# Kernel optimization log

Hardware: AMD Instinct MI355X
Metric: run time of the kernel (lower is better)

Reference implementation:

```python
import jax, jax.numpy as jnp
import numpy as np

DX = 1.0
DY = 1.0
W_DIV = 1e9
W_SMOOTH = 10.0
W_STD = 100.0
EPS = 1e-10


def _corner(a, i, j, k):
    # slice dims 2,3,4: 0 -> [0:-1], 1 -> [1:]
    sl = lambda b: slice(1, None) if b else slice(0, -1)
    return a[:, :, sl(i), sl(j), sl(k)]


def setup_inputs() -> dict:
    key = jax.random.key(0)
    k1, k2 = jax.random.split(key)
    outputs = jax.random.normal(k1, (2, 1, 256, 256, 64), dtype=jnp.float32)
    targets = jax.random.normal(k2, (2, 3, 256, 256, 64), dtype=jnp.float32)
    return {"outputs": outputs, "targets": targets}


def _loss(outputs, targets):
    bx, by, bz = targets[:, 0:1], targets[:, 1:2], targets[:, 2:3]
    z = outputs[:, 0:1]

    # vertical thickness and smoothness of its square
    dz = z[..., 1:] - z[..., :-1]
    dz2 = dz ** 2
    lap = (6 * dz2[:, :, 1:-1, 1:-1, 1:-1]
           - dz2[:, :, :-2, 1:-1, 1:-1] - dz2[:, :, 2:, 1:-1, 1:-1]
           - dz2[:, :, 1:-1, :-2, 1:-1] - dz2[:, :, 1:-1, 2:, 1:-1]
           - dz2[:, :, 1:-1, 1:-1, 2:] - dz2[:, :, 1:-1, 1:-1, :-2])
    loss_smooth = jnp.mean(lap ** 2)

    # per-(batch, channel, z) std over the spatial plane (unbiased, matching torch.std)
    loss_std = jnp.mean(jnp.std(dz, axis=(2, 3), ddof=1))

    # 8 cell corners for each field
    corners = lambda a: {(i, j, k): _corner(a, i, j, k)
                         for i in (0, 1) for j in (0, 1) for k in (0, 1)}
    BX, BY, BZ, Z = corners(bx), corners(by), corners(bz), corners(z)

    az = lambda a, b: jnp.abs(Z[a] - Z[b])
    num = (0.25 * (BX[1,0,0] + BX[1,1,0] + BX[1,0,1] + BX[1,1,1]) * DY * 0.5 * (az((1,0,1),(1,0,0)) + az((1,1,1),(1,1,0)))
           - 0.25 * (BX[0,0,0] + BX[0,1,0] + BX[0,0,1] + BX[0,1,1]) * DY * 0.5 * (az((0,0,1),(0,0,0)) + az((0,1,1),(0,1,0)))
           + 0.25 * (BY[0,1,0] + BY[1,1,0] + BY[0,1,1] + BY[1,1,1]) * DX * 0.5 * (az((0,1,1),(0,1,0)) + az((1,1,1),(1,1,0)))
           - 0.25 * (BY[0,0,0] + BY[1,0,0] + BY[0,0,1] + BY[1,0,1]) * DX * 0.5 * (az((0,0,1),(0,0,0)) + az((1,0,1),(1,0,0)))
           + 0.25 * (BZ[0,0,1] + BZ[0,1,1] + BZ[1,0,1] + BZ[1,1,1]) * DX * DY
           - 0.25 * (BZ[0,0,0] + BZ[0,1,0] + BZ[1,0,0] + BZ[1,1,0]) * DX * DY
           + (BX[0,0,1] + BX[1,0,1] + BX[1,1,1]) * DY * (Z[0,0,1] - Z[1,0,1]) / 6
           + (BX[0,1,1] + BX[1,1,1] + BX[1,0,1]) * DY * (Z[0,1,1] - Z[1,1,1]) / 6
           + (BY[1,0,1] + BY[1,1,1] + BY[0,1,1]) * DX * (Z[1,0,1] - Z[1,1,1]) / 6
           + (BY[0,0,1] + BY[0,1,1] + BY[1,1,1]) * DX * (Z[0,0,1] - Z[0,1,1]) / 6
           - (BX[0,0,0] + BX[1,0,0] + BX[1,1,0]) * DY * (Z[0,0,0] - Z[1,0,0]) / 6
           - (BX[0,1,0] + BX[1,1,0] + BX[1,0,0]) * DY * (Z[0,1,0] - Z[1,1,0]) / 6
           - (BY[1,0,0] + BY[1,1,0] + BY[0,1,0]) * DX * (Z[1,0,0] - Z[1,1,0]) / 6
           - (BY[0,0,0] + BY[0,1,0] + BY[1,1,0]) * DX * (Z[0,0,0] - Z[0,1,0]) / 6)

    sum8 = lambda C: sum(C.values())
    den = ((sum8(BX) * 0.125) ** 2 + (sum8(BY) * 0.125) ** 2
           + (sum8(BZ) * 0.125) ** 2 + EPS)
    loss_div = jnp.mean(num ** 2 / den)

    return loss_div * W_DIV, loss_smooth * W_SMOOTH + loss_std * W_STD


def reference(outputs, targets):
    return _loss(outputs, targets)
```

## Files before the change

### kernel.cpp

```cpp
#include <hip/hip_runtime.h>
#include <math.h>


#define ZSTR 388
#define BSTR 324
#define BFLD 1620

__global__ __launch_bounds__(512) void zero_ws_kernel(float* ws) {
    for (int i = threadIdx.x; i < 32 * 258; i += 512) ws[i] = 0.0f;
}

#define LD5(arr, p) do { \
    float4 _a = *(const float4*)(p); float4 _b = *(const float4*)((p) + 4); \
    arr[0] = _a.x; arr[1] = _a.y; arr[2] = _a.z; arr[3] = _a.w; arr[4] = _b.x; } while (0)

__global__ __launch_bounds__(256, 4) void fused_loss_kernel(
    const float* __restrict__ zin, const float* __restrict__ tg,
    float* __restrict__ ws)
{
    __shared__ float zs[6 * ZSTR];
    __shared__ float bs[3 * BFLD];
    __shared__ float rsc[4][2];

    const int tid  = threadIdx.x;
    const int lane = tid & 63;
    const int w    = tid >> 6;

    const int bb = blockIdx.x >> 12;
    const int rest = blockIdx.x & 4095;
    const int x0 = ((rest >> 6) & 63) << 2;
    const int y0 = (rest & 63) << 2;

    const float* zg = zin + ((size_t)bb << 22);

    for (int i = tid; i < 1776; i += 256) {
        if (i < 576) {
            int row = i >> 4;
            int o   = (i & 15) << 2;
            int xi  = row / 6;
            int yr  = row - xi * 6;
            int x = x0 - 1 + xi; x = x < 0 ? 0 : (x > 255 ? 255 : x);
            int y = y0 - 1 + yr; y = y < 0 ? 0 : (y > 255 ? 255 : y);
            *(float4*)&zs[xi * ZSTR + yr * 64 + o] =
                *(const float4*)&zg[x * 16384 + y * 64 + o];
        } else {
            int j  = i - 576;
            int f  = j / 400;
            int jj = j - f * 400;
            int row = jj >> 4;
            int o   = (jj & 15) << 2;
            int xi  = row / 5;
            int yr  = row - xi * 5;
            int x = x0 + xi; x = x > 255 ? 255 : x;
            int y = y0 + yr; y = y > 255 ? 255 : y;
            const float* g = tg + ((size_t)(bb * 3 + f) << 22);
            *(float4*)&bs[f * BFLD + xi * BSTR + yr * 64 + o] =
                *(const float4*)&g[x * 16384 + y * 64 + o];
        }
    }
    __syncthreads();

    const int c  = tid >> 4;
    const int kq = tid & 15;
    const int cx = c & 3, cy = c >> 2;
    const int xg = x0 + cx, yg = y0 + cy;
    const int k0 = kq << 2;

    const float* zC = &zs[(cx + 1) * ZSTR + (cy + 1) * 64 + k0];

    float zcv[7];
    {
        float4 m = *(const float4*)(zC - 4);
        float4 a = *(const float4*)(zC);
        float4 b = *(const float4*)(zC + 4);
        zcv[0] = m.w; zcv[1] = a.x; zcv[2] = a.y; zcv[3] = a.z; zcv[4] = a.w;
        zcv[5] = b.x; zcv[6] = b.y;
    }
    float zEv[5];  LD5(zEv,  zC + ZSTR);
    float zWv[5];  LD5(zWv,  zC - ZSTR);
    float zNv[5];  LD5(zNv,  zC + 64);
    float zSv[5];  LD5(zSv,  zC - 64);
    float zNEv[5]; LD5(zNEv, zC + ZSTR + 64);

    float dz0[4], dzE[4], dzN[4], dzNE[4];
    #pragma unroll
    for (int e = 0; e < 4; ++e) {
        dz0[e]  = zcv[e + 2] - zcv[e + 1];
        dzE[e]  = zEv[e + 1] - zEv[e];
        dzN[e]  = zNv[e + 1] - zNv[e];
        dzNE[e] = zNEv[e + 1] - zNEv[e];
    }

    float s1a[4], s2a[4];
    #pragma unroll
    for (int e = 0; e < 4; ++e) {
        bool kok = (k0 + e) < 63;
        s1a[e] = kok ? dz0[e] : 0.0f;
        s2a[e] = kok ? dz0[e] * dz0[e] : 0.0f;
    }

    float sm = 0.0f;
    if (xg >= 1 && xg <= 254 && yg >= 1 && yg <= 254) {
        #pragma unroll
        for (int e = 0; e < 4; ++e) {
            int k = k0 + e;
            if (k >= 1 && k <= 61) {
                float dzm = zcv[e + 1] - zcv[e];
                float dzp = zcv[e + 3] - zcv[e + 2];
                float dzw = zWv[e + 1] - zWv[e];
                float dzs = zSv[e + 1] - zSv[e];
                float lap = 6.0f * dz0[e] * dz0[e]
                          - dzw * dzw - dzE[e] * dzE[e]
                          - dzs * dzs - dzN[e] * dzN[e]
                          - dzm * dzm - dzp * dzp;
                sm += lap * lap;
            }
        }
    }

    float dv = 0.0f;
    if (xg < 255 && yg < 255) {
        const float* bxP = &bs[cx * BSTR + cy * 64 + k0];
        const float* byP = bxP + BFLD;
        const float* bzP = byP + BFLD;
        float bx00v[5]; LD5(bx00v, bxP);
        float bx10v[5]; LD5(bx10v, bxP + BSTR);
        float bx01v[5]; LD5(bx01v, bxP + 64);
        float bx11v[5]; LD5(bx11v, bxP + BSTR + 64);
        float by00v[5]; LD5(by00v, byP);
        float by10v[5]; LD5(by10v, byP + BSTR);
        float by01v[5]; LD5(by01v, byP + 64);
        float by11v[5]; LD5(by11v, byP + BSTR + 64);
        float bz00v[5]; LD5(bz00v, bzP);
        float bz10v[5]; LD5(bz10v, bzP + BSTR);
        float bz01v[5]; LD5(bz01v, bzP + 64);
        float bz11v[5]; LD5(bz11v, bzP + BSTR + 64);

        const float c6 = 1.0f / 6.0f;
        #pragma unroll
        for (int e = 0; e < 4; ++e) {
            if ((k0 + e) < 63) {
                float adz00 = fabsf(dz0[e]),  adz10 = fabsf(dzE[e]);
                float adz01 = fabsf(dzN[e]),  adz11 = fabsf(dzNE[e]);

                float num =
                    0.125f * ( (bx10v[e] + bx10v[e+1] + bx11v[e] + bx11v[e+1]) * (adz10 + adz11)
                             - (bx00v[e] + bx00v[e+1] + bx01v[e] + bx01v[e+1]) * (adz00 + adz01)
                             + (by01v[e] + by01v[e+1] + by11v[e] + by11v[e+1]) * (adz01 + adz11)
                             - (by00v[e] + by00v[e+1] + by10v[e] + by10v[e+1]) * (adz00 + adz10) )
                  + 0.25f * ( (bz00v[e+1] + bz10v[e+1] + bz01v[e+1] + bz11v[e+1])
                            - (bz00v[e]   + bz10v[e]   + bz01v[e]   + bz11v[e]) );

                num += c6 * ( (bx00v[e+1] + bx10v[e+1] + bx11v[e+1]) * (zcv[e+2] - zEv[e+1])
                            + (bx01v[e+1] + bx11v[e+1] + bx10v[e+1]) * (zNv[e+1] - zNEv[e+1])
                            + (by10v[e+1] + by11v[e+1] + by01v[e+1]) * (zEv[e+1] - zNEv[e+1])
                            + (by00v[e+1] + by01v[e+1] + by11v[e+1]) * (zcv[e+2] - zNv[e+1])
                            - (bx00v[e] + bx10v[e] + bx11v[e]) * (zcv[e+1] - zEv[e])
                            - (bx01v[e] + bx11v[e] + bx10v[e]) * (zNv[e] - zNEv[e])
                            - (by10v[e] + by11v[e] + by01v[e]) * (zEv[e] - zNEv[e])
                            - (by00v[e] + by01v[e] + by11v[e]) * (zcv[e+1] - zNv[e]) );

                float sbx = bx00v[e] + bx00v[e+1] + bx10v[e] + bx10v[e+1]
                          + bx01v[e] + bx01v[e+1] + bx11v[e] + bx11v[e+1];
                float sby = by00v[e] + by00v[e+1] + by10v[e] + by10v[e+1]
                          + by01v[e] + by01v[e+1] + by11v[e] + by11v[e+1];
                float sbz = bz00v[e] + bz00v[e+1] + bz10v[e] + bz10v[e+1]
                          + bz01v[e] + bz01v[e+1] + bz11v[e] + bz11v[e+1];
                float den = 0.015625f * (sbx * sbx + sby * sby + sbz * sbz) + 1e-10f;
                dv += num * num / den;
            }
        }
    }

    #pragma unroll
    for (int off = 32; off > 0; off >>= 1) {
        sm += __shfl_down(sm, off, 64);
        dv += __shfl_down(dv, off, 64);
    }

    __syncthreads();
    float* r1 = zs;
    float* r2 = zs + 1024;
    { float4 v; v.x = s1a[0]; v.y = s1a[1]; v.z = s1a[2]; v.w = s1a[3];
      *(float4*)&r1[tid << 2] = v; }
    { float4 v; v.x = s2a[0]; v.y = s2a[1]; v.z = s2a[2]; v.w = s2a[3];
      *(float4*)&r2[tid << 2] = v; }
    if (lane == 0) { rsc[w][0] = sm; rsc[w][1] = dv; }
    __syncthreads();

    if (tid < 64) {
        float a = 0.0f, b2 = 0.0f;
        #pragma unroll
        for (int cc = 0; cc < 16; ++cc) {
            a  += r1[cc * 64 + tid];
            b2 += r2[cc * 64 + tid];
        }
        float* sl = ws + (blockIdx.x & 31) * 258;
        if (tid < 63) {
            atomicAdd(&sl[2 + bb * 64 + tid],   a);
            atomicAdd(&sl[130 + bb * 64 + tid], b2);
        }
        if (tid == 0) atomicAdd(&sl[0], rsc[0][0] + rsc[1][0] + rsc[2][0] + rsc[3][0]);
        if (tid == 1) atomicAdd(&sl[1], rsc[0][1] + rsc[1][1] + rsc[2][1] + rsc[3][1]);
    }
}

__global__ __launch_bounds__(128) void finalize_kernel(const float* __restrict__ ws,
                                                       float* __restrict__ out)
{
    __shared__ double red[128];
    const int t = threadIdx.x;
    double stdv = 0.0;
    {
        int k = t & 63, bb = t >> 6;
        if (k < 63) {
            double s1 = 0.0, s2 = 0.0;
            for (int p = 0; p < 32; ++p) {
                s1 += (double)ws[p * 258 + 2 + bb * 64 + k];
                s2 += (double)ws[p * 258 + 130 + bb * 64 + k];
            }
            const double N = 65536.0;
            double var = (s2 - s1 * s1 / N) / (N - 1.0);
            stdv = sqrt(var > 0.0 ? var : 0.0);
        }
    }
    red[t] = stdv;
    __syncthreads();
    for (int off = 64; off > 0; off >>= 1) {
        if (t < off) red[t] += red[t + off];
        __syncthreads();
    }
    if (t == 0) {
        double smt = 0.0, dvt = 0.0;
        for (int p = 0; p < 32; ++p) {
            smt += (double)ws[p * 258 + 0];
            dvt += (double)ws[p * 258 + 1];
        }
        double loss_std    = red[0] / 126.0;
        double loss_smooth = smt / (2.0 * 254.0 * 254.0 * 61.0);
        double loss_div    = dvt / (2.0 * 255.0 * 255.0 * 63.0);
        out[0] = (float)(loss_div * 1e9);
        out[1] = (float)(loss_smooth * 10.0 + loss_std * 100.0);
    }
}

extern "C" void kernel_launch(void* const* d_in, const int* in_sizes, int n_in,
                              void* d_out, int out_size, void* d_ws, size_t ws_size,
                              hipStream_t stream) {
    const float* z  = (const float*)d_in[0];
    const float* tg = (const float*)d_in[1];
    float* out = (float*)d_out;
    float* ws  = (float*)d_ws;

    zero_ws_kernel<<<1, 512, 0, stream>>>(ws);
    fused_loss_kernel<<<8192, 256, 0, stream>>>(z, tg, ws);
    finalize_kernel<<<1, 128, 0, stream>>>(ws, out);
}
```

Before: 206.8 us.

## Load stencil neighbours directly from global memory instead of staging tiles in LDS

Drops the shared-memory tile staging pass and its barrier. Each thread now reads its z neighbours and B-field corners straight from global memory with clamped indices, relying on L1/L2 to serve the overlapping reads. The divergence computation is split into per-field stages to cut live registers, and the divide becomes a hardware reciprocal approximation. This removes LDS traffic and a sync, but adds redundant global loads and slightly less exact division.

Measured after the change: 210.9 us. About the same (+2.0%).

```diff
diff --git a/kernel.cpp b/kernel.cpp
--- a/kernel.cpp
+++ b/kernel.cpp
@@ -2,85 +2,69 @@
 #include <math.h>
 
 
-#define ZSTR 388
-#define BSTR 324
-#define BFLD 1620
-
 __global__ __launch_bounds__(512) void zero_ws_kernel(float* ws) {
     for (int i = threadIdx.x; i < 32 * 258; i += 512) ws[i] = 0.0f;
 }
 
-#define LD5(arr, p) do { \
-    float4 _a = *(const float4*)(p); float4 _b = *(const float4*)((p) + 4); \
-    arr[0] = _a.x; arr[1] = _a.y; arr[2] = _a.z; arr[3] = _a.w; arr[4] = _b.x; } while (0)
+__device__ __forceinline__ void ld5(float* a, const float* p, int d4) {
+    float4 x = *(const float4*)p;
+    float4 y = *(const float4*)(p + d4);
+    a[0] = x.x; a[1] = x.y; a[2] = x.z; a[3] = x.w; a[4] = y.x;
+}
 
 __global__ __launch_bounds__(256, 4) void fused_loss_kernel(
     const float* __restrict__ zin, const float* __restrict__ tg,
     float* __restrict__ ws)
 {
-    __shared__ float zs[6 * ZSTR];
-    __shared__ float bs[3 * BFLD];
+    __shared__ float r1[1024];
+    __shared__ float r2[1024];
     __shared__ float rsc[4][2];
 
     const int tid  = threadIdx.x;
     const int lane = tid & 63;
     const int w    = tid >> 6;
 
-    const int bb = blockIdx.x >> 12;
+    const int bb   = blockIdx.x >> 12;
     const int rest = blockIdx.x & 4095;
     const int x0 = ((rest >> 6) & 63) << 2;
     const int y0 = (rest & 63) << 2;
-
-    const float* zg = zin + ((size_t)bb << 22);
-
-    for (int i = tid; i < 1776; i += 256) {
-        if (i < 576) {
-            int row = i >> 4;
-            int o   = (i & 15) << 2;
-            int xi  = row / 6;
-            int yr  = row - xi * 6;
-            int x = x0 - 1 + xi; x = x < 0 ? 0 : (x > 255 ? 255 : x);
-            int y = y0 - 1 + yr; y = y < 0 ? 0 : (y > 255 ? 255 : y);
-            *(float4*)&zs[xi * ZSTR + yr * 64 + o] =
-                *(const float4*)&zg[x * 16384 + y * 64 + o];
-        } else {
-            int j  = i - 576;
-            int f  = j / 400;
-            int jj = j - f * 400;
-            int row = jj >> 4;
-            int o   = (jj & 15) << 2;
-            int xi  = row / 5;
-            int yr  = row - xi * 5;
-            int x = x0 + xi; x = x > 255 ? 255 : x;
-            int y = y0 + yr; y = y > 255 ? 255 : y;
-            const float* g = tg + ((size_t)(bb * 3 + f) << 22);
-            *(float4*)&bs[f * BFLD + xi * BSTR + yr * 64 + o] =
-                *(const float4*)&g[x * 16384 + y * 64 + o];
-        }
-    }
-    __syncthreads();
 
     const int c  = tid >> 4;
     const int kq = tid & 15;
     const int cx = c & 3, cy = c >> 2;
     const int xg = x0 + cx, yg = y0 + cy;
     const int k0 = kq << 2;
-
-    const float* zC = &zs[(cx + 1) * ZSTR + (cy + 1) * 64 + k0];
+    const int d4 = (kq < 15) ? 4 : 0;
+
+    const int xE = (xg < 255) ? xg + 1 : 255;
+    const int xW = (xg > 0)   ? xg - 1 : 0;
+    const int yN = (yg < 255) ? yg + 1 : 255;
+    const int yS = (yg > 0)   ? yg - 1 : 0;
+
+    const int oC  = xg * 16384 + yg * 64 + k0;
+    const int oE  = xE * 16384 + yg * 64 + k0;
+    const int oW  = xW * 16384 + yg * 64 + k0;
+    const int oN  = xg * 16384 + yN * 64 + k0;
+    const int oS  = xg * 16384 + yS * 64 + k0;
+    const int oNE = xE * 16384 + yN * 64 + k0;
+
+    const float* zg = zin + ((size_t)bb << 22);
 
     float zcv[7];
     {
-        float4 m = *(const float4*)(zC - 4);
-        float4 a = *(const float4*)(zC);
-        float4 b = *(const float4*)(zC + 4);
+        int km = (k0 >= 4) ? -4 : 0;
+        float4 m = *(const float4*)&zg[oC + km];
+        float4 a = *(const float4*)&zg[oC];
+        float4 b = *(const float4*)&zg[oC + d4];
         zcv[0] = m.w; zcv[1] = a.x; zcv[2] = a.y; zcv[3] = a.z; zcv[4] = a.w;
         zcv[5] = b.x; zcv[6] = b.y;
     }
-    float zEv[5];  LD5(zEv,  zC + ZSTR);
-    float zWv[5];  LD5(zWv,  zC - ZSTR);
-    float zNv[5];  LD5(zNv,  zC + 64);
-    float zSv[5];  LD5(zSv,  zC - 64);
-    float zNEv[5]; LD5(zNEv, zC + ZSTR + 64);
+    float zEv[5], zWv[5], zNv[5], zSv[5], zNEv[5];
+    ld5(zEv,  &zg[oE],  d4);
+    ld5(zWv,  &zg[oW],  d4);
+    ld5(zNv,  &zg[oN],  d4);
+    ld5(zSv,  &zg[oS],  d4);
+    ld5(zNEv, &zg[oNE], d4);
 
     float dz0[4], dzE[4], dzN[4], dzNE[4];
     #pragma unroll
@@ -90,7 +74,6 @@
         dzN[e]  = zNv[e + 1] - zNv[e];
         dzNE[e] = zNEv[e + 1] - zNEv[e];
     }
-
     float s1a[4], s2a[4];
     #pragma unroll
     for (int e = 0; e < 4; ++e) {
@@ -120,54 +103,83 @@
 
     float dv = 0.0f;
     if (xg < 255 && yg < 255) {
-        const float* bxP = &bs[cx * BSTR + cy * 64 + k0];
-        const float* byP = bxP + BFLD;
-        const float* bzP = byP + BFLD;
-        float bx00v[5]; LD5(bx00v, bxP);
-        float bx10v[5]; LD5(bx10v, bxP + BSTR);
-        float bx01v[5]; LD5(bx01v, bxP + 64);
-        float bx11v[5]; LD5(bx11v, bxP + BSTR + 64);
-        float by00v[5]; LD5(by00v, byP);
-        float by10v[5]; LD5(by10v, byP + BSTR);
-        float by01v[5]; LD5(by01v, byP + 64);
-        float by11v[5]; LD5(by11v, byP + BSTR + 64);
-        float bz00v[5]; LD5(bz00v, bzP);
-        float bz10v[5]; LD5(bz10v, bzP + BSTR);
-        float bz01v[5]; LD5(bz01v, bzP + 64);
-        float bz11v[5]; LD5(bz11v, bzP + BSTR + 64);
-
+        float dCE[5], dCN[5], dENE[5], dNNE[5];
+        #pragma unroll
+        for (int j = 0; j < 5; ++j) {
+            dCE[j]  = zcv[j + 1] - zEv[j];
+            dCN[j]  = zcv[j + 1] - zNv[j];
+            dENE[j] = zEv[j] - zNEv[j];
+            dNNE[j] = zNv[j] - zNEv[j];
+        }
+        float adz00[4], adz10[4], adz01[4], adz11[4];
+        #pragma unroll
+        for (int e = 0; e < 4; ++e) {
+            adz00[e] = fabsf(dz0[e]);  adz10[e] = fabsf(dzE[e]);
+            adz01[e] = fabsf(dzN[e]);  adz11[e] = fabsf(dzNE[e]);
+        }
+
+        const int p00 = oC, p10 = oE, p01 = oN, p11 = oNE;
+        const float* bxg = tg + ((size_t)(bb * 3) << 22);
+        const float* byg = bxg + (1u << 22);
+        const float* bzg = byg + (1u << 22);
         const float c6 = 1.0f / 6.0f;
+
+        float num[4], den[4];
+
+        {
+            float a00[5], a10[5], a01[5], a11[5];
+            ld5(a00, &bxg[p00], d4);  ld5(a10, &bxg[p10], d4);
+            ld5(a01, &bxg[p01], d4);  ld5(a11, &bxg[p11], d4);
+            #pragma unroll
+            for (int e = 0; e < 4; ++e) {
+                float s10 = a10[e] + a10[e + 1] + a11[e] + a11[e + 1];
+                float s00 = a00[e] + a00[e + 1] + a01[e] + a01[e + 1];
+                num[e] = 0.125f * (s10 * (adz10[e] + adz11[e])
+                                 - s00 * (adz00[e] + adz01[e]));
+                num[e] += c6 * ( (a00[e + 1] + a10[e + 1] + a11[e + 1]) * dCE[e + 1]
+                               + (a01[e + 1] + a11[e + 1] + a10[e + 1]) * dNNE[e + 1]
+                               - (a00[e] + a10[e] + a11[e]) * dCE[e]
+                               - (a01[e] + a11[e] + a10[e]) * dNNE[e] );
+                float sbx = s10 + s00;
+                den[e] = sbx * sbx;
+            }
+        }
+        {
+            float a00[5], a10[5], a01[5], a11[5];
+            ld5(a00, &byg[p00], d4);  ld5(a10, &byg[p10], d4);
+            ld5(a01, &byg[p01], d4);  ld5(a11, &byg[p11], d4);
+            #pragma unroll
+            for (int e = 0; e < 4; ++e) {
+                float s01 = a01[e] + a01[e + 1] + a11[e] + a11[e + 1];
+                float s00 = a00[e] + a00[e + 1] + a10[e] + a10[e + 1];
+                num[e] += 0.125f * (s01 * (adz01[e] + adz11[e])
+                                  - s00 * (adz00[e] + adz10[e]));
+                num[e] += c6 * ( (a10[e + 1] + a11[e + 1] + a01[e + 1]) * dENE[e + 1]
+                               + (a00[e + 1] + a01[e + 1] + a11[e + 1]) * dCN[e + 1]
+                               - (a10[e] + a11[e] + a01[e]) * dENE[e]
+                               - (a00[e] + a01[e] + a11[e]) * dCN[e] );
+                float sby = s01 + s00;
+                den[e] += sby * sby;
+            }
+        }
+        {
+            float a00[5], a10[5], a01[5], a11[5];
+            ld5(a00, &bzg[p00], d4);  ld5(a10, &bzg[p10], d4);
+            ld5(a01, &bzg[p01], d4);  ld5(a11, &bzg[p11], d4);
+            #pragma unroll
+            for (int e = 0; e < 4; ++e) {
+                float slo = a00[e] + a10[e] + a01[e] + a11[e];
+                float shi = a00[e + 1] + a10[e + 1] + a01[e + 1] + a11[e + 1];
+                num[e] += 0.25f * (shi - slo);
+                float sbz = slo + shi;
+                den[e] += sbz * sbz;
+            }
+        }
         #pragma unroll
         for (int e = 0; e < 4; ++e) {
             if ((k0 + e) < 63) {
-                float adz00 = fabsf(dz0[e]),  adz10 = fabsf(dzE[e]);
-                float adz01 = fabsf(dzN[e]),  adz11 = fabsf(dzNE[e]);
-
-                float num =
-                    0.125f * ( (bx10v[e] + bx10v[e+1] + bx11v[e] + bx11v[e+1]) * (adz10 + adz11)
-                             - (bx00v[e] + bx00v[e+1] + bx01v[e] + bx01v[e+1]) * (adz00 + adz01)
-                             + (by01v[e] + by01v[e+1] + by11v[e] + by11v[e+1]) * (adz01 + adz11)
-                             - (by00v[e] + by00v[e+1] + by10v[e] + by10v[e+1]) * (adz00 + adz10) )
-                  + 0.25f * ( (bz00v[e+1] + bz10v[e+1] + bz01v[e+1] + bz11v[e+1])
-                            - (bz00v[e]   + bz10v[e]   + bz01v[e]   + bz11v[e]) );
-
-                num += c6 * ( (bx00v[e+1] + bx10v[e+1] + bx11v[e+1]) * (zcv[e+2] - zEv[e+1])
-                            + (bx01v[e+1] + bx11v[e+1] + bx10v[e+1]) * (zNv[e+1] - zNEv[e+1])
-                            + (by10v[e+1] + by11v[e+1] + by01v[e+1]) * (zEv[e+1] - zNEv[e+1])
-                            + (by00v[e+1] + by01v[e+1] + by11v[e+1]) * (zcv[e+2] - zNv[e+1])
-                            - (bx00v[e] + bx10v[e] + bx11v[e]) * (zcv[e+1] - zEv[e])
-                            - (bx01v[e] + bx11v[e] + bx10v[e]) * (zNv[e] - zNEv[e])
-                            - (by10v[e] + by11v[e] + by01v[e]) * (zEv[e] - zNEv[e])
-                            - (by00v[e] + by01v[e] + by11v[e]) * (zcv[e+1] - zNv[e]) );
-
-                float sbx = bx00v[e] + bx00v[e+1] + bx10v[e] + bx10v[e+1]
-                          + bx01v[e] + bx01v[e+1] + bx11v[e] + bx11v[e+1];
-                float sby = by00v[e] + by00v[e+1] + by10v[e] + by10v[e+1]
-                          + by01v[e] + by01v[e+1] + by11v[e] + by11v[e+1];
-                float sbz = bz00v[e] + bz00v[e+1] + bz10v[e] + bz10v[e+1]
-                          + bz01v[e] + bz01v[e+1] + bz11v[e] + bz11v[e+1];
-                float den = 0.015625f * (sbx * sbx + sby * sby + sbz * sbz) + 1e-10f;
-                dv += num * num / den;
+                float d = den[e] * 0.015625f + 1e-10f;
+                dv += num[e] * num[e] * __builtin_amdgcn_rcpf(d);
             }
         }
     }
@@ -178,9 +190,6 @@
         dv += __shfl_down(dv, off, 64);
     }
 
-    __syncthreads();
-    float* r1 = zs;
-    float* r2 = zs + 1024;
     { float4 v; v.x = s1a[0]; v.y = s1a[1]; v.z = s1a[2]; v.w = s1a[3];
       *(float4*)&r1[tid << 2] = v; }
     { float4 v; v.x = s2a[0]; v.y = s2a[1]; v.z = s2a[2]; v.w = s2a[3];
```
